# Kernel optimization log

Hardware: AMD Instinct MI355X
Metric: run time of the kernel (lower is better)

The kernel has to match this reference:

```python
import jax, jax.numpy as jnp
import numpy as np

N_NODES = 100000
N_EDGES = 3200000  # avg degree 32
D_IN = 128
D_OUT = 64


def setup_inputs() -> dict:
    key = jax.random.key(0)
    k1, k2, k3, k4, k5 = jax.random.split(key, 5)
    h = jax.random.normal(k1, (N_NODES, D_IN), dtype=jnp.float32)
    W = jax.random.normal(k2, (D_IN, D_OUT), dtype=jnp.float32) / np.float32(np.sqrt(D_IN))
    a = jax.random.normal(k3, (2 * D_OUT,), dtype=jnp.float32) / np.float32(np.sqrt(2 * D_OUT))
    src = jax.random.randint(k4, (N_EDGES,), 0, N_NODES, dtype=jnp.int32)
    dst = jax.random.randint(k5, (N_EDGES,), 0, N_NODES, dtype=jnp.int32)
    return {"h": h, "W": W, "a": a, "src": src, "dst": dst}


def reference(h, W, a, src, dst):
    N = h.shape[0]
    d = W.shape[1]
    # node projection: z = linear(h)  (bias-free, n_mlp_layer=1)
    z = h @ W  # [N, d]
    # edge attention logit: attn_linear(cat([z_src, z_dst])) == z_src@a[:d] + z_dst@a[d:]
    e = z[src] @ a[:d] + z[dst] @ a[d:]  # [E]
    # segment softmax over incoming edges of each destination node
    m = jax.ops.segment_max(e, dst, num_segments=N)  # [N]
    w = jnp.exp(e - m[dst])  # [E]
    s = jax.ops.segment_sum(w, dst, num_segments=N)  # [N]
    alpha = w / s[dst]  # [E]
    # weighted scatter-sum of source features (nodes with no in-edges stay 0, as in DGL)
    out = jax.ops.segment_sum(alpha[:, None] * z[src], dst, num_segments=N)  # [N, d]
    return out
```

## Files before the change

kernel.cpp:

```cpp
#include <hip/hip_runtime.h>

#define D_IN 128
#define D_OUT 64
#define SCAN_ITEMS 2048
#define TILE 8192
#define BSHIFT 7
#define NBK 128
#define MAXNB 1024
#define CAP 8192
#define BN 64
#define HS_STRIDE 132
#define MAXSB 1024
#define PROJ_LDS (D_IN * D_OUT + BN * HS_STRIDE)

typedef float f32x4 __attribute__((ext_vector_type(4)));
typedef int   i32x4 __attribute__((ext_vector_type(4)));

__device__ __forceinline__ unsigned short f32_to_bf16(float f) {
    unsigned int u = __float_as_uint(f);
    u += 0x7fffu + ((u >> 16) & 1u);
    return (unsigned short)(u >> 16);
}

__device__ __forceinline__ void proj_body512(
    float* ws, float* hs,
    const float* __restrict__ h, const float* __restrict__ W,
    const float* __restrict__ a, unsigned short* __restrict__ z16,
    float* __restrict__ E, int n_nodes, int blk, int tid)
{
    const int nbase = blk * BN;

#pragma unroll
    for (int i = 0; i < 4; ++i) {
        int f = (tid + 512 * i) * 4;
        *(float4*)&ws[f] = *(const float4*)&W[f];
    }
#pragma unroll
    for (int j = 0; j < 4; ++j) {
        int f = tid + 512 * j;
        int row = f >> 5;
        int kk = (f & 31) << 2;
        int gr = nbase + row;
        float4 v = make_float4(0.f, 0.f, 0.f, 0.f);
        if (gr < n_nodes) v = *(const float4*)&h[(size_t)gr * D_IN + kk];
        *(float4*)&hs[row * HS_STRIDE + kk] = v;
    }
    __syncthreads();

    const int c4 = (tid & 15) * 4;
    const int n2 = (tid >> 4) * 2;

    float acc[2][4];
#pragma unroll
    for (int i = 0; i < 2; ++i)
#pragma unroll
        for (int j = 0; j < 4; ++j) acc[i][j] = 0.0f;

    for (int k = 0; k < D_IN; k += 4) {
        float4 wv0 = *(float4*)&ws[(k + 0) * D_OUT + c4];
        float4 wv1 = *(float4*)&ws[(k + 1) * D_OUT + c4];
        float4 wv2 = *(float4*)&ws[(k + 2) * D_OUT + c4];
        float4 wv3 = *(float4*)&ws[(k + 3) * D_OUT + c4];
#pragma unroll
        for (int i = 0; i < 2; ++i) {
            float4 hv = *(float4*)&hs[(n2 + i) * HS_STRIDE + k];
            acc[i][0] = fmaf(hv.x, wv0.x, acc[i][0]);
            acc[i][1] = fmaf(hv.x, wv0.y, acc[i][1]);
            acc[i][2] = fmaf(hv.x, wv0.z, acc[i][2]);
            acc[i][3] = fmaf(hv.x, wv0.w, acc[i][3]);
            acc[i][0] = fmaf(hv.y, wv1.x, acc[i][0]);
            acc[i][1] = fmaf(hv.y, wv1.y, acc[i][1]);
            acc[i][2] = fmaf(hv.y, wv1.z, acc[i][2]);
            acc[i][3] = fmaf(hv.y, wv1.w, acc[i][3]);
            acc[i][0] = fmaf(hv.z, wv2.x, acc[i][0]);
            acc[i][1] = fmaf(hv.z, wv2.y, acc[i][1]);
            acc[i][2] = fmaf(hv.z, wv2.z, acc[i][2]);
            acc[i][3] = fmaf(hv.z, wv2.w, acc[i][3]);
            acc[i][0] = fmaf(hv.w, wv3.x, acc[i][0]);
            acc[i][1] = fmaf(hv.w, wv3.y, acc[i][1]);
            acc[i][2] = fmaf(hv.w, wv3.z, acc[i][2]);
            acc[i][3] = fmaf(hv.w, wv3.w, acc[i][3]);
        }
    }

    float a0 = a[c4 + 0], a1 = a[c4 + 1], a2 = a[c4 + 2], a3 = a[c4 + 3];
#pragma unroll
    for (int i = 0; i < 2; ++i) {
        int node = nbase + n2 + i;
        bool ok = node < n_nodes;
        if (ok) {
            ushort4 q;
            q.x = f32_to_bf16(acc[i][0]);
            q.y = f32_to_bf16(acc[i][1]);
            q.z = f32_to_bf16(acc[i][2]);
            q.w = f32_to_bf16(acc[i][3]);
            *(ushort4*)&z16[(size_t)node * D_OUT + c4] = q;
        }
        float es_p = acc[i][0] * a0 + acc[i][1] * a1 + acc[i][2] * a2 + acc[i][3] * a3;
        es_p += __shfl_xor(es_p, 1, 64);
        es_p += __shfl_xor(es_p, 2, 64);
        es_p += __shfl_xor(es_p, 4, 64);
        es_p += __shfl_xor(es_p, 8, 64);
        if ((tid & 15) == 0 && ok)
            E[node] = __expf(fminf(fmaxf(es_p, -60.0f), 60.0f));
    }
}

__global__ __launch_bounds__(512) void k_project(
    const float* __restrict__ h, const float* __restrict__ W,
    const float* __restrict__ a, unsigned short* __restrict__ z16,
    float* __restrict__ E, int n_nodes)
{
    __shared__ float smem[PROJ_LDS];
    proj_body512(smem, smem + D_IN * D_OUT, h, W, a, z16, E, n_nodes,
                 blockIdx.x, threadIdx.x);
}

__global__ __launch_bounds__(512) void k_hist2(
    const int* __restrict__ dst, unsigned int* __restrict__ btot,
    int n_edges, int NB)
{
    __shared__ unsigned int hcnt[MAXNB];
    int t = blockIdx.x;
    for (int b = threadIdx.x; b < NB; b += 512) hcnt[b] = 0;
    __syncthreads();
    int base = t * TILE;
    int lim = min(base + TILE, n_edges);
    for (int i = base + threadIdx.x * 4; i < lim; i += 2048) {
        if (i + 4 <= lim) {
            i32x4 d4 = __builtin_nontemporal_load((const i32x4*)&dst[i]);
            atomicAdd(&hcnt[(unsigned int)d4.x >> BSHIFT], 1u);
            atomicAdd(&hcnt[(unsigned int)d4.y >> BSHIFT], 1u);
            atomicAdd(&hcnt[(unsigned int)d4.z >> BSHIFT], 1u);
            atomicAdd(&hcnt[(unsigned int)d4.w >> BSHIFT], 1u);
        } else {
            for (int k = i; k < lim; ++k)
                atomicAdd(&hcnt[(unsigned int)dst[k] >> BSHIFT], 1u);
        }
    }
    __syncthreads();
    for (int b = threadIdx.x; b < NB; b += 512) {
        unsigned int c = hcnt[b];
        if (c) atomicAdd(&btot[b], c);
    }
}

__global__ __launch_bounds__(256) void k_bscan(
    const unsigned int* __restrict__ btot, unsigned int* __restrict__ boff,
    unsigned int* __restrict__ gcur, int nb)
{
    __shared__ unsigned int tmp[256];
    int tid = threadIdx.x;
    unsigned int v[8]; unsigned int tsum = 0;
#pragma unroll
    for (int j = 0; j < 8; ++j) {
        int idx = tid * 8 + j;
        v[j] = (idx < nb) ? btot[idx] : 0u;
        tsum += v[j];
    }
    tmp[tid] = tsum; __syncthreads();
    for (int o = 1; o < 256; o <<= 1) {
        unsigned int u = (tid >= o) ? tmp[tid - o] : 0u; __syncthreads();
        tmp[tid] += u; __syncthreads();
    }
    unsigned int run = tmp[tid] - tsum;
#pragma unroll
    for (int j = 0; j < 8; ++j) {
        int idx = tid * 8 + j;
        if (idx < nb) { boff[idx] = run; gcur[idx] = run; }
        run += v[j];
    }
    if (tid == 255) boff[nb] = tmp[255];
}

__global__ __launch_bounds__(512) void k_proj_part(
    const float* __restrict__ h, const float* __restrict__ W,
    const float* __restrict__ a, unsigned short* __restrict__ z16,
    float* __restrict__ E,
    const int* __restrict__ src, const int* __restrict__ dst,
    unsigned int* __restrict__ gcur, unsigned int* __restrict__ tmp,
    int n_nodes, int n_edges, int NPT, int NB)
{
    __shared__ float smem[PROJ_LDS];
    const int tid = threadIdx.x;

    if ((int)blockIdx.x < NPT) {
        unsigned int* cnt = (unsigned int*)smem;
        const int t = blockIdx.x;
        const int base = t * TILE;
        const int lim = min(base + TILE, n_edges);

        for (int b = tid; b < NB; b += 512) cnt[b] = 0;
        __syncthreads();

        unsigned int dv[16], sv[16];
#pragma unroll
        for (int j = 0; j < 4; ++j) {
            int i = base + tid * 4 + j * 2048;
            if (i + 4 <= lim) {
                i32x4 d4 = __builtin_nontemporal_load((const i32x4*)&dst[i]);
                i32x4 s4 = __builtin_nontemporal_load((const i32x4*)&src[i]);
                dv[4 * j + 0] = (unsigned int)d4.x; sv[4 * j + 0] = (unsigned int)s4.x;
                dv[4 * j + 1] = (unsigned int)d4.y; sv[4 * j + 1] = (unsigned int)s4.y;
                dv[4 * j + 2] = (unsigned int)d4.z; sv[4 * j + 2] = (unsigned int)s4.z;
                dv[4 * j + 3] = (unsigned int)d4.w; sv[4 * j + 3] = (unsigned int)s4.w;
            } else {
#pragma unroll
                for (int k = 0; k < 4; ++k) {
                    int ii = i + k;
                    bool ok = ii < lim;
                    dv[4 * j + k] = ok ? (unsigned int)dst[ii] : 0xFFFFFFFFu;
                    sv[4 * j + k] = ok ? (unsigned int)src[ii] : 0u;
                }
            }
        }

#pragma unroll
        for (int k = 0; k < 16; ++k) {
            unsigned int d = dv[k];
            if (d != 0xFFFFFFFFu) atomicAdd(&cnt[d >> BSHIFT], 1u);
        }
        __syncthreads();

        for (int b = tid; b < NB; b += 512) {
            unsigned int c = cnt[b];
            cnt[b] = c ? atomicAdd(&gcur[b], c) : 0u;
        }
        __syncthreads();

#pragma unroll
        for (int k = 0; k < 16; ++k) {
            unsigned int d = dv[k];
            if (d != 0xFFFFFFFFu) {
                unsigned int pos = atomicAdd(&cnt[d >> BSHIFT], 1u);
                tmp[pos] = (sv[k] << BSHIFT) | (d & (NBK - 1u));
            }
        }
    } else {
        proj_body512(smem, smem + D_IN * D_OUT, h, W, a, z16, E, n_nodes,
                     blockIdx.x - NPT, tid);
    }
}

__global__ __launch_bounds__(512) void k_gather(
    const unsigned int* __restrict__ tmp, const unsigned int* __restrict__ boff,
    const float* __restrict__ E, const unsigned short* __restrict__ z16,
    int* __restrict__ sscratch, float* __restrict__ out,
    int n_edges, int n_nodes, int NB)
{
    __shared__ unsigned int offL[NBK + 1];
    __shared__ unsigned int cnt[NBK];
    __shared__ unsigned int sedge[CAP];

    const int b = blockIdx.x;
    const int tid = threadIdx.x;
    const unsigned int s0 = boff[b];
    const unsigned int s1 = boff[b + 1];
    const unsigned int sz = s1 - s0;
    const bool inLds = (sz <= CAP);

    unsigned int ev[16];
    if (inLds) {
#pragma unroll
        for (int j = 0; j < 16; ++j) {
            unsigned int i = s0 + (unsigned int)tid + 512u * (unsigned int)j;
            ev[j] = (i < s1) ? __builtin_nontemporal_load(&tmp[i]) : 0u;
        }
    }

    if (tid < NBK) cnt[tid] = 0;
    __syncthreads();
    if (inLds) {
#pragma unroll
        for (int j = 0; j < 16; ++j) {
            unsigned int i = s0 + (unsigned int)tid + 512u * (unsigned int)j;
            if (i < s1) atomicAdd(&cnt[ev[j] & (NBK - 1u)], 1u);
        }
    } else {
        for (unsigned int i = s0 + tid; i < s1; i += 512)
            atomicAdd(&cnt[tmp[i] & (NBK - 1u)], 1u);
    }
    __syncthreads();

    if (tid < 64) {
        unsigned int c0 = cnt[2 * tid], c1 = cnt[2 * tid + 1];
        unsigned int ps = c0 + c1;
        unsigned int run = ps;
#pragma unroll
        for (int o = 1; o < 64; o <<= 1) {
            unsigned int u = __shfl_up(run, o, 64);
            if (tid >= o) run += u;
        }
        unsigned int excl = run - ps;
        offL[2 * tid]     = excl;
        offL[2 * tid + 1] = excl + c0;
        cnt[2 * tid]      = excl;
        cnt[2 * tid + 1]  = excl + c0;
        if (tid == 63) offL[NBK] = run;
    }
    __syncthreads();

    if (inLds) {
#pragma unroll
        for (int j = 0; j < 16; ++j) {
            unsigned int i = s0 + (unsigned int)tid + 512u * (unsigned int)j;
            if (i < s1) {
                unsigned int val = ev[j];
                unsigned int pos = atomicAdd(&cnt[val & (NBK - 1u)], 1u);
                sedge[pos] = val >> BSHIFT;
            }
        }
    } else {
        for (unsigned int i = s0 + tid; i < s1; i += 512) {
            unsigned int val = tmp[i];
            unsigned int pos = atomicAdd(&cnt[val & (NBK - 1u)], 1u);
            sscratch[s0 + pos] = (int)(val >> BSHIFT);
        }
    }
    __syncthreads();

    const int wave = tid >> 6;
    const int lane = tid & 63;
    const int g = lane >> 3;
    const int fl = lane & 7;

    for (int dl = wave; dl < NBK; dl += 8) {
        int node = (b << BSHIFT) + dl;
        if (node >= n_nodes) break;
        unsigned int a0 = offL[dl], a1 = offL[dl + 1];
        float* orow = out + (size_t)node * D_OUT;
        if (a0 == a1) {
            if (g == 0) {
                __builtin_nontemporal_store((f32x4)0.f, (f32x4*)(orow + fl * 8));
                __builtin_nontemporal_store((f32x4)0.f, (f32x4*)(orow + fl * 8 + 4));
            }
            continue;
        }

        float acc[8];
#pragma unroll
        for (int j = 0; j < 8; ++j) acc[j] = 0.0f;
        float wsum = 0.0f;

        unsigned int i = a0 + (unsigned int)g;
        if (inLds) {
            for (; i + 8 < a1; i += 16) {
                int sn0 = (int)sedge[i];
                int sn1 = (int)sedge[i + 8];
                float w0 = E[sn0];
                float w1 = E[sn1];
                uint4 p0 = *(const uint4*)(z16 + (size_t)sn0 * D_OUT + fl * 8);
                uint4 p1 = *(const uint4*)(z16 + (size_t)sn1 * D_OUT + fl * 8);
                wsum += w0 + w1;
                const unsigned int pu0[4] = {p0.x, p0.y, p0.z, p0.w};
                const unsigned int pu1[4] = {p1.x, p1.y, p1.z, p1.w};
#pragma unroll
                for (int q = 0; q < 4; ++q) {
                    acc[2 * q]     = fmaf(w0, __uint_as_float(pu0[q] << 16),         acc[2 * q]);
                    acc[2 * q + 1] = fmaf(w0, __uint_as_float(pu0[q] & 0xffff0000u), acc[2 * q + 1]);
                    acc[2 * q]     = fmaf(w1, __uint_as_float(pu1[q] << 16),         acc[2 * q]);
                    acc[2 * q + 1] = fmaf(w1, __uint_as_float(pu1[q] & 0xffff0000u), acc[2 * q + 1]);
                }
            }
            if (i < a1) {
                int sn = (int)sedge[i];
                float w = E[sn];
                const uint4 p = *(const uint4*)(z16 + (size_t)sn * D_OUT + fl * 8);
                wsum += w;
                const unsigned int pu[4] = {p.x, p.y, p.z, p.w};
#pragma unroll
                for (int q = 0; q < 4; ++q) {
                    acc[2 * q]     = fmaf(w, __uint_as_float(pu[q] << 16),         acc[2 * q]);
                    acc[2 * q + 1] = fmaf(w, __uint_as_float(pu[q] & 0xffff0000u), acc[2 * q + 1]);
                }
            }
        } else {
            for (; i < a1; i += 8) {
                int sn = sscratch[s0 + i];
                float w = E[sn];
                const uint4 p = *(const uint4*)(z16 + (size_t)sn * D_OUT + fl * 8);
                wsum += w;
                const unsigned int pu[4] = {p.x, p.y, p.z, p.w};
#pragma unroll
                for (int q = 0; q < 4; ++q) {
                    acc[2 * q]     = fmaf(w, __uint_as_float(pu[q] << 16),         acc[2 * q]);
                    acc[2 * q + 1] = fmaf(w, __uint_as_float(pu[q] & 0xffff0000u), acc[2 * q + 1]);
                }
            }
        }

#pragma unroll
        for (int o = 8; o <= 32; o <<= 1) {
#pragma unroll
            for (int j = 0; j < 8; ++j) acc[j] += __shfl_xor(acc[j], o, 64);
            wsum += __shfl_xor(wsum, o, 64);
        }

        if (g == 0) {
            float inv = __builtin_amdgcn_rcpf(wsum);
            f32x4 o0 = {acc[0] * inv, acc[1] * inv, acc[2] * inv, acc[3] * inv};
            f32x4 o1 = {acc[4] * inv, acc[5] * inv, acc[6] * inv, acc[7] * inv};
            __builtin_nontemporal_store(o0, (f32x4*)(orow + fl * 8));
            __builtin_nontemporal_store(o1, (f32x4*)(orow + fl * 8 + 4));
        }
    }
}

__global__ __launch_bounds__(256) void k_rank(
    const int* __restrict__ dst, unsigned int* __restrict__ count,
    unsigned short* __restrict__ rank, int n_edges)
{
    int e = blockIdx.x * blockDim.x + threadIdx.x;
    if (e < n_edges) rank[e] = (unsigned short)atomicAdd(&count[dst[e]], 1u);
}

__global__ __launch_bounds__(256) void k_place(
    const int* __restrict__ src, const int* __restrict__ dst,
    const unsigned int* __restrict__ off, const unsigned short* __restrict__ rank,
    int* __restrict__ ssrc, int n_edges)
{
    int e = blockIdx.x * blockDim.x + threadIdx.x;
    if (e < n_edges) ssrc[off[dst[e]] + (unsigned int)rank[e]] = src[e];
}

__global__ __launch_bounds__(256) void k_count(
    const int* __restrict__ dst, unsigned int* __restrict__ count, int n_edges)
{
    int e = blockIdx.x * blockDim.x + threadIdx.x;
    if (e < n_edges) atomicAdd(&count[dst[e]], 1u);
}

__global__ __launch_bounds__(256) void k_fill(
    const int* __restrict__ src, const int* __restrict__ dst,
    unsigned int* __restrict__ cursor, int* __restrict__ ssrc, int n_edges)
{
    int e = blockIdx.x * blockDim.x + threadIdx.x;
    if (e < n_edges) {
        unsigned int pos = atomicAdd(&cursor[dst[e]], 1u);
        ssrc[pos] = src[e];
    }
}

__global__ __launch_bounds__(256) void k_fused(
    const int* __restrict__ ssrc, const unsigned int* __restrict__ off,
    const float* __restrict__ E, const unsigned short* __restrict__ z16,
    float* __restrict__ out, int n_nodes)
{
    int node = (blockIdx.x * blockDim.x + threadIdx.x) >> 6;
    int lane = threadIdx.x & 63;
    if (node >= n_nodes) return;
    int g  = lane >> 3;
    int fl = lane & 7;

    unsigned int start = off[node], end = off[node + 1];
    float* orow = out + (size_t)node * D_OUT;
    if (start == end) {
        if (g == 0) {
            *(float4*)(orow + fl * 8)     = make_float4(0.f, 0.f, 0.f, 0.f);
            *(float4*)(orow + fl * 8 + 4) = make_float4(0.f, 0.f, 0.f, 0.f);
        }
        return;
    }

    float acc[8];
#pragma unroll
    for (int j = 0; j < 8; ++j) acc[j] = 0.0f;
    float wsum = 0.0f;

    for (unsigned int i = start + g; i < end; i += 8) {
        int sn = ssrc[i];
        float w = E[sn];
        wsum += w;
        const uint4 p = *(const uint4*)(z16 + (size_t)sn * D_OUT + fl * 8);
        const unsigned int pu[4] = {p.x, p.y, p.z, p.w};
#pragma unroll
        for (int q = 0; q < 4; ++q) {
            float lo = __uint_as_float(pu[q] << 16);
            float hi = __uint_as_float(pu[q] & 0xffff0000u);
            acc[2 * q]     = fmaf(w, lo, acc[2 * q]);
            acc[2 * q + 1] = fmaf(w, hi, acc[2 * q + 1]);
        }
    }

#pragma unroll
    for (int o = 8; o <= 32; o <<= 1) {
#pragma unroll
        for (int j = 0; j < 8; ++j) acc[j] += __shfl_xor(acc[j], o, 64);
        wsum += __shfl_xor(wsum, o, 64);
    }

    if (g == 0) {
        float inv = 1.0f / wsum;
        float4 o0 = make_float4(acc[0] * inv, acc[1] * inv, acc[2] * inv, acc[3] * inv);
        float4 o1 = make_float4(acc[4] * inv, acc[5] * inv, acc[6] * inv, acc[7] * inv);
        *(float4*)(orow + fl * 8)     = o0;
        *(float4*)(orow + fl * 8 + 4) = o1;
    }
}

__global__ __launch_bounds__(256) void k_scan1(
    const unsigned int* __restrict__ count, unsigned int* __restrict__ off,
    unsigned int* __restrict__ blk_sums, int n)
{
    __shared__ unsigned int tmp[256];
    int tid = threadIdx.x;
    int base = blockIdx.x * SCAN_ITEMS;
    unsigned int v[8]; unsigned int tsum = 0;
#pragma unroll
    for (int i = 0; i < 8; ++i) {
        int idx = base + tid * 8 + i;
        v[i] = (idx < n) ? count[idx] : 0u;
        tsum += v[i];
    }
    tmp[tid] = tsum; __syncthreads();
    for (int o = 1; o < 256; o <<= 1) {
        unsigned int u = (tid >= o) ? tmp[tid - o] : 0u; __syncthreads();
        tmp[tid] += u; __syncthreads();
    }
    unsigned int run = tmp[tid] - tsum;
    if (tid == 255) blk_sums[blockIdx.x] = tmp[255];
#pragma unroll
    for (int i = 0; i < 8; ++i) {
        int idx = base + tid * 8 + i;
        if (idx < n) off[idx] = run;
        run += v[i];
    }
}

__global__ __launch_bounds__(256) void k_scan2(
    const unsigned int* __restrict__ blk_sums, unsigned int* __restrict__ blk_offs,
    unsigned int* __restrict__ off, int nblocks, int n)
{
    __shared__ unsigned int tmp[256];
    int tid = threadIdx.x;
    unsigned int carry = 0;
    for (int base = 0; base < nblocks; base += 256) {
        unsigned int v = (base + tid < nblocks) ? blk_sums[base + tid] : 0u;
        tmp[tid] = v; __syncthreads();
        for (int o = 1; o < 256; o <<= 1) {
            unsigned int u = (tid >= o) ? tmp[tid - o] : 0u; __syncthreads();
            tmp[tid] += u; __syncthreads();
        }
        if (base + tid < nblocks) blk_offs[base + tid] = carry + tmp[tid] - v;
        carry += tmp[255];
        __syncthreads();
    }
    if (tid == 0) off[n] = carry;
}

__global__ __launch_bounds__(256) void k_scan3(
    unsigned int* __restrict__ off, unsigned int* __restrict__ cursor,
    const unsigned int* __restrict__ blk_offs, int n)
{
    int i = blockIdx.x * blockDim.x + threadIdx.x;
    if (i < n) {
        unsigned int o = off[i] + blk_offs[i / SCAN_ITEMS];
        off[i] = o; cursor[i] = o;
    }
}

extern "C" void kernel_launch(void* const* d_in, const int* in_sizes, int n_in,
                              void* d_out, int out_size, void* d_ws, size_t ws_size,
                              hipStream_t stream) {
    const float* h   = (const float*)d_in[0];
    const float* W   = (const float*)d_in[1];
    const float* a   = (const float*)d_in[2];
    const int*   src = (const int*)d_in[3];
    const int*   dst = (const int*)d_in[4];
    float* out = (float*)d_out;

    const int n_nodes = in_sizes[0] / D_IN;
    const int n_edges = in_sizes[3];

    const int NB = (n_nodes + NBK - 1) >> BSHIFT;
    const int NPT = (n_edges + TILE - 1) / TILE;
    const int PB = (n_nodes + BN - 1) / BN;

    auto align = [](size_t x) { return (x + 255) & ~(size_t)255; };
    char* w = (char*)d_ws;
    unsigned short* z16 = (unsigned short*)w;  w += align((size_t)n_nodes * D_OUT * sizeof(unsigned short));
    float* E = (float*)w;                      w += align((size_t)n_nodes * sizeof(float));
    unsigned int* off = (unsigned int*)w;      w += align(((size_t)n_nodes + 1) * sizeof(unsigned int));
    unsigned int* blk_sums = (unsigned int*)w; w += align(MAXSB * sizeof(unsigned int));
    unsigned int* blk_offs = (unsigned int*)w; w += align(MAXSB * sizeof(unsigned int));
    size_t hist_elems = (size_t)n_nodes > 8192 ? (size_t)n_nodes : (size_t)8192;
    unsigned int* histT = (unsigned int*)w;    w += align(hist_elems * sizeof(unsigned int));
    unsigned int* btot = histT;
    unsigned int* boff = histT + 2048;
    unsigned int* gcur = histT + 4352;
    unsigned int* count = histT;
    int* ssrc = (int*)w;                       w += align((size_t)n_edges * sizeof(int));
    unsigned int* tmp = (unsigned int*)w;
    unsigned short* rank = (unsigned short*)tmp;
    size_t need_sort = ((char*)tmp - (char*)d_ws) + align((size_t)n_edges * sizeof(unsigned int));
    size_t need_rank = ((char*)tmp - (char*)d_ws) + align((size_t)n_edges * sizeof(unsigned short));

    const bool use_sort = (ws_size >= need_sort) && NB <= MAXNB &&
                          n_nodes < (1 << 25);
    const bool use_rank = !use_sort && (ws_size >= need_rank);

    const int eblocks = (n_edges + 255) / 256;
    const int sb_node = (n_nodes + SCAN_ITEMS - 1) / SCAN_ITEMS;

    if (use_sort) {
        hipMemsetAsync(btot, 0, (size_t)(NB + 1) * sizeof(unsigned int), stream);
        k_hist2<<<NPT, 512, 0, stream>>>(dst, btot, n_edges, NB);
        k_bscan<<<1, 256, 0, stream>>>(btot, boff, gcur, NB);
        k_proj_part<<<NPT + PB, 512, 0, stream>>>(h, W, a, z16, E, src, dst,
                                                  gcur, tmp, n_nodes, n_edges,
                                                  NPT, NB);
        k_gather<<<NB, 512, 0, stream>>>(tmp, boff, E, z16, ssrc, out,
                                         n_edges, n_nodes, NB);
    } else if (use_rank) {
        k_project<<<PB, 512, 0, stream>>>(h, W, a, z16, E, n_nodes);
        hipMemsetAsync(count, 0, (size_t)n_nodes * sizeof(unsigned int), stream);
        k_rank<<<eblocks, 256, 0, stream>>>(dst, count, rank, n_edges);
        k_scan1<<<sb_node, 256, 0, stream>>>(count, off, blk_sums, n_nodes);
        k_scan2<<<1, 256, 0, stream>>>(blk_sums, blk_offs, off, sb_node, n_nodes);
        k_scan3<<<(n_nodes + 255) / 256, 256, 0, stream>>>(off, count, blk_offs, n_nodes);
        k_place<<<eblocks, 256, 0, stream>>>(src, dst, off, rank, ssrc, n_edges);
        k_fused<<<(n_nodes + 3) / 4, 256, 0, stream>>>(ssrc, off, E, z16, out, n_nodes);
    } else {
        k_project<<<PB, 512, 0, stream>>>(h, W, a, z16, E, n_nodes);
        hipMemsetAsync(count, 0, (size_t)n_nodes * sizeof(unsigned int), stream);
        k_count<<<eblocks, 256, 0, stream>>>(dst, count, n_edges);
        k_scan1<<<sb_node, 256, 0, stream>>>(count, off, blk_sums, n_nodes);
        k_scan2<<<1, 256, 0, stream>>>(blk_sums, blk_offs, off, sb_node, n_nodes);
        k_scan3<<<(n_nodes + 255) / 256, 256, 0, stream>>>(off, count, blk_offs, n_nodes);
        k_fill<<<eblocks, 256, 0, stream>>>(src, dst, count, ssrc, n_edges);
        k_fused<<<(n_nodes + 3) / 4, 256, 0, stream>>>(ssrc, off, E, z16, out, n_nodes);
    }
}
```

Before: 236.9 us.

## Split node projection across histogram and partition kernels, shrink histogram tiles

Fuses the destination-bucket histogram kernel with the first half of the node projection blocks, so the dense GEMV-like work overlaps the atomic-heavy histogram pass. The remaining half of the projection stays in the partition kernel, offset by a new base index. Histogram tiles shrink from 8192 to 2048 edges per block, which gives more blocks and more parallelism but also more global atomics on the bucket totals. Histogram blocks now carry the large projection LDS allocation, which may lower their occupancy.

```diff
diff --git a/kernel.cpp b/kernel.cpp
--- a/kernel.cpp
+++ b/kernel.cpp
@@ -4,6 +4,7 @@
 #define D_OUT 64
 #define SCAN_ITEMS 2048
 #define TILE 8192
+#define TILE_H 2048
 #define BSHIFT 7
 #define NBK 128
 #define MAXNB 1024
@@ -116,32 +117,43 @@
                  blockIdx.x, threadIdx.x);
 }
 
-__global__ __launch_bounds__(512) void k_hist2(
-    const int* __restrict__ dst, unsigned int* __restrict__ btot,
-    int n_edges, int NB)
-{
-    __shared__ unsigned int hcnt[MAXNB];
-    int t = blockIdx.x;
-    for (int b = threadIdx.x; b < NB; b += 512) hcnt[b] = 0;
-    __syncthreads();
-    int base = t * TILE;
-    int lim = min(base + TILE, n_edges);
-    for (int i = base + threadIdx.x * 4; i < lim; i += 2048) {
-        if (i + 4 <= lim) {
-            i32x4 d4 = __builtin_nontemporal_load((const i32x4*)&dst[i]);
-            atomicAdd(&hcnt[(unsigned int)d4.x >> BSHIFT], 1u);
-            atomicAdd(&hcnt[(unsigned int)d4.y >> BSHIFT], 1u);
-            atomicAdd(&hcnt[(unsigned int)d4.z >> BSHIFT], 1u);
-            atomicAdd(&hcnt[(unsigned int)d4.w >> BSHIFT], 1u);
-        } else {
-            for (int k = i; k < lim; ++k)
-                atomicAdd(&hcnt[(unsigned int)dst[k] >> BSHIFT], 1u);
-        }
-    }
-    __syncthreads();
-    for (int b = threadIdx.x; b < NB; b += 512) {
-        unsigned int c = hcnt[b];
-        if (c) atomicAdd(&btot[b], c);
+__global__ __launch_bounds__(512) void k_proj_hist(
+    const float* __restrict__ h, const float* __restrict__ W,
+    const float* __restrict__ a, unsigned short* __restrict__ z16,
+    float* __restrict__ E, const int* __restrict__ dst,
+    unsigned int* __restrict__ btot,
+    int n_nodes, int n_edges, int NHT, int NB)
+{
+    __shared__ float smem[PROJ_LDS];
+    const int tid = threadIdx.x;
+
+    if ((int)blockIdx.x < NHT) {
+        unsigned int* hcnt = (unsigned int*)smem;
+        const int t = blockIdx.x;
+        for (int b = tid; b < NB; b += 512) hcnt[b] = 0;
+        __syncthreads();
+        int base = t * TILE_H;
+        int lim = min(base + TILE_H, n_edges);
+        for (int i = base + tid * 4; i < lim; i += 2048) {
+            if (i + 4 <= lim) {
+                i32x4 d4 = __builtin_nontemporal_load((const i32x4*)&dst[i]);
+                atomicAdd(&hcnt[(unsigned int)d4.x >> BSHIFT], 1u);
+                atomicAdd(&hcnt[(unsigned int)d4.y >> BSHIFT], 1u);
+                atomicAdd(&hcnt[(unsigned int)d4.z >> BSHIFT], 1u);
+                atomicAdd(&hcnt[(unsigned int)d4.w >> BSHIFT], 1u);
+            } else {
+                for (int k2 = i; k2 < lim; ++k2)
+                    atomicAdd(&hcnt[(unsigned int)dst[k2] >> BSHIFT], 1u);
+            }
+        }
+        __syncthreads();
+        for (int b = tid; b < NB; b += 512) {
+            unsigned int c = hcnt[b];
+            if (c) atomicAdd(&btot[b], c);
+        }
+    } else {
+        proj_body512(smem, smem + D_IN * D_OUT, h, W, a, z16, E, n_nodes,
+                     blockIdx.x - NHT, tid);
     }
 }
 
@@ -179,7 +191,7 @@
     float* __restrict__ E,
     const int* __restrict__ src, const int* __restrict__ dst,
     unsigned int* __restrict__ gcur, unsigned int* __restrict__ tmp,
-    int n_nodes, int n_edges, int NPT, int NB)
+    int n_nodes, int n_edges, int NPT, int NB, int proj_base)
 {
     __shared__ float smem[PROJ_LDS];
     const int tid = threadIdx.x;
@@ -238,7 +250,7 @@
         }
     } else {
         proj_body512(smem, smem + D_IN * D_OUT, h, W, a, z16, E, n_nodes,
-                     blockIdx.x - NPT, tid);
+                     proj_base + (int)blockIdx.x - NPT, tid);
     }
 }
 
@@ -574,7 +586,10 @@
 
     const int NB = (n_nodes + NBK - 1) >> BSHIFT;
     const int NPT = (n_edges + TILE - 1) / TILE;
+    const int NHT = (n_edges + TILE_H - 1) / TILE_H;
     const int PB = (n_nodes + BN - 1) / BN;
+    const int PH1 = (PB + 1) / 2;
+    const int PH2 = PB - PH1;
 
     auto align = [](size_t x) { return (x + 255) & ~(size_t)255; };
     char* w = (char*)d_ws;
@@ -604,11 +619,12 @@
 
     if (use_sort) {
         hipMemsetAsync(btot, 0, (size_t)(NB + 1) * sizeof(unsigned int), stream);
-        k_hist2<<<NPT, 512, 0, stream>>>(dst, btot, n_edges, NB);
+        k_proj_hist<<<NHT + PH1, 512, 0, stream>>>(h, W, a, z16, E, dst, btot,
+                                                   n_nodes, n_edges, NHT, NB);
         k_bscan<<<1, 256, 0, stream>>>(btot, boff, gcur, NB);
-        k_proj_part<<<NPT + PB, 512, 0, stream>>>(h, W, a, z16, E, src, dst,
-                                                  gcur, tmp, n_nodes, n_edges,
-                                                  NPT, NB);
+        k_proj_part<<<NPT + PH2, 512, 0, stream>>>(h, W, a, z16, E, src, dst,
+                                                   gcur, tmp, n_nodes, n_edges,
+                                                   NPT, NB, PH1);
         k_gather<<<NB, 512, 0, stream>>>(tmp, boff, E, z16, ssrc, out,
                                          n_edges, n_nodes, NB);
     } else if (use_rank) {
```

Result: slower. 263.5 us (+11.2%).
